# Kernel tuning notes

Measured on AMD Instinct MI355X. Metric: run time of the kernel, lower is better.

Reference implementation:

```python
import jax, jax.numpy as jnp
import numpy as np

B = 1048576          # batch size
ALPHA1, ALPHA2, ALPHA3 = 1.2566, 1.5, 0.9
S_STAR = 20.0
TAU = 4.0


def _f_matrix(a1, a2, a3):
    # fixed 6x6 dynamics matrix built by the i in {1,2} loop in CBF_Parameters
    f = jnp.zeros((6, 6), jnp.float32)
    f = f.at[2, 1].set(1.0).at[2, 3].set(-1.0)
    f = f.at[3, 1].set(a3).at[3, 2].set(a1).at[3, 3].set(-a2)
    f = f.at[4, 3].set(1.0).at[4, 5].set(-1.0)
    f = f.at[5, 3].set(a3).at[5, 4].set(a1).at[5, 5].set(-a2)
    return f


def setup_inputs() -> dict:
    key = jax.random.key(0)
    ks = jax.random.split(key, 7)
    z = jax.random.normal(ks[0], (B, 6), jnp.float32)
    tilde_vh = jnp.zeros((1,), jnp.float32)  # unused in forward (dead code in source)
    W1 = jax.random.normal(ks[1], (50, 6), jnp.float32) * 0.3
    b1 = jax.random.normal(ks[2], (50,), jnp.float32) * 0.1
    W2 = jax.random.normal(ks[3], (100, 50), jnp.float32) * 0.1
    b2 = jax.random.normal(ks[4], (100,), jnp.float32) * 0.1
    W3 = jax.random.normal(ks[5], (5, 100), jnp.float32) * 0.1
    b3 = jax.random.normal(ks[6], (5,), jnp.float32) * 0.1
    return dict(z=z, tilde_vh=tilde_vh, W1=W1, b1=b1, W2=W2, b2=b2, W3=W3, b3=b3)


def reference(z, tilde_vh, W1, b1, W2, b2, W3, b3):
    # tiny MLP, no activations (faithful to fc3(fc2(fc1(z))))
    u = ((z @ W1.T + b1) @ W2.T + b2) @ W3.T + b3        # (B, 5)
    p1, p2, p3 = u[:, 1], u[:, 2], u[:, 3]

    # faithful: torch reshape (row-major reinterpret), not transpose
    X = z.reshape(6, -1)                                  # (6, B)
    f = _f_matrix(ALPHA1, ALPHA2, ALPHA3)
    fX = f @ X                                            # (6, B)

    # index == 2 constraint (while loop body never runs: delta_b[1]=tau != 0)
    d2 = jnp.zeros(6, jnp.float32).at[1].set(TAU).at[2].set(1.0).at[3].set(-TAU)
    eta1 = X[2] + S_STAR - TAU * (X[3] - X[1])            # (B,)
    bb1 = d2 @ fX + p1 * eta1                             # (B,)

    # index == 3 constraint (while loop runs exactly once: d3[1]==0 -> d3u[1]=tau*alpha3)
    d3 = jnp.zeros(6, jnp.float32).at[3].set(TAU).at[4].set(1.0).at[5].set(-TAU)
    d3u = d3 @ f                                          # one f-multiplication
    eta2a = X[4] + S_STAR - TAU * (X[5] - X[3])           # (B,)
    eta2b = d3u @ X                                       # (B,)
    bb2 = d3u @ fX + p2 * eta2a + p3 * eta2b              # (B,)

    A = jnp.stack([-d2[1], -d3u[1]])                      # (2,) constraint normals
    h = jnp.stack([bb1, bb2], axis=1)                     # (B, 2)

    # per-sample 1-D QP: min 0.25*x^2 - u0*x  s.t. A_i * x <= h_i  (Q = 0.5)
    x_unc = 2.0 * u[:, 0]
    ratios = h / A                                        # (B, 2)
    neg_inf = jnp.float32(-1e30)
    pos_inf = jnp.float32(1e30)
    lb = jnp.max(jnp.where(A < 0, ratios, neg_inf), axis=1)
    ub = jnp.min(jnp.where(A > 0, ratios, pos_inf), axis=1)
    return jnp.clip(x_unc, lb, ub)[:, None]               # (B, 1)
```

## Files before the change

### kernel.cpp

```cpp
#include <hip/hip_runtime.h>

#define ALPHA1 1.2566f
#define ALPHA2 1.5f
#define ALPHA3 0.9f
#define S_STAR 20.0f
#define TAU    4.0f

constexpr int TPB = 256;

__global__ __launch_bounds__(TPB) void fused_kernel(
        const float* __restrict__ z,
        const float* __restrict__ W1, const float* __restrict__ b1,
        const float* __restrict__ W2, const float* __restrict__ b2,
        const float* __restrict__ W3, const float* __restrict__ b3,
        float* __restrict__ out, long long B) {
    __shared__ float Vs[4][52];
    __shared__ float Ms[4][6];
    __shared__ float cs[4];
    const int tid = threadIdx.x;

    if (tid < 200) {
        const int m = tid / 50, h = tid % 50;
        float s = 0.f;
        #pragma unroll 10
        for (int i = 0; i < 100; ++i)
            s = fmaf(W3[m * 100 + i], W2[i * 50 + h], s);
        Vs[m][h] = s;
    }
    __syncthreads();
    if (tid < 24) {
        const int m = tid / 6, k = tid % 6;
        float s = 0.f;
        #pragma unroll 10
        for (int h = 0; h < 50; ++h)
            s = fmaf(Vs[m][h], W1[h * 6 + k], s);
        Ms[m][k] = s;
    } else if (tid < 28) {
        const int m = tid - 24;
        float s = b3[m];
        #pragma unroll 10
        for (int i = 0; i < 100; ++i)
            s = fmaf(W3[m * 100 + i], b2[i], s);
        #pragma unroll 10
        for (int h = 0; h < 50; ++h)
            s = fmaf(Vs[m][h], b1[h], s);
        cs[m] = s;
    }
    __syncthreads();

    float M[4][6], c[4];
    #pragma unroll
    for (int m = 0; m < 4; ++m) {
        #pragma unroll
        for (int k = 0; k < 6; ++k) M[m][k] = Ms[m][k];
        c[m] = cs[m];
    }

    const float g1 = TAU * ALPHA3;
    const float g2 = TAU * ALPHA1;
    const float g3 = 1.f - TAU * ALPHA2 - TAU * ALPHA3;
    const float g4 = -TAU * ALPHA1;
    const float g5 = TAU * ALPHA2 - 1.f;

    #pragma unroll
    for (int s2 = 0; s2 < 2; ++s2) {
        const long long j0 =
            ((long long)blockIdx.x * (2 * TPB) + s2 * TPB + tid) * 4;

        float zz[24];
        const float4* zr = (const float4*)(z + j0 * 6);
        #pragma unroll
        for (int v = 0; v < 6; ++v) {
            const float4 q = zr[v];
            zz[4 * v + 0] = q.x; zz[4 * v + 1] = q.y;
            zz[4 * v + 2] = q.z; zz[4 * v + 3] = q.w;
        }

        float X[6][4];
        #pragma unroll
        for (int i = 0; i < 6; ++i) {
            const float4 q = *(const float4*)(z + (long long)i * B + j0);
            X[i][0] = q.x; X[i][1] = q.y; X[i][2] = q.z; X[i][3] = q.w;
        }

        float4 o;
        float* op = &o.x;
        #pragma unroll
        for (int r = 0; r < 4; ++r) {
            float u[4];
            #pragma unroll
            for (int m = 0; m < 4; ++m) {
                float s = c[m];
                #pragma unroll
                for (int k = 0; k < 6; ++k) s = fmaf(M[m][k], zz[r * 6 + k], s);
                u[m] = s;
            }
            const float x1 = X[1][r], x2 = X[2][r], x3 = X[3][r];
            const float x4 = X[4][r], x5 = X[5][r];

            const float fx2 = x1 - x3;
            const float fx3 = ALPHA3 * x1 + ALPHA1 * x2 - ALPHA2 * x3;
            const float fx4 = x3 - x5;
            const float fx5 = ALPHA3 * x3 + ALPHA1 * x4 - ALPHA2 * x5;

            const float eta1 = x2 + S_STAR - TAU * (x3 - x1);
            const float bb1  = (fx2 - TAU * fx3) + u[1] * eta1;

            const float eta2a = x4 + S_STAR - TAU * (x5 - x3);
            const float eta2b = g1 * x1 + g2 * x2 + g3 * x3 + g4 * x4 + g5 * x5;
            const float d3ufX = g2 * fx2 + g3 * fx3 + g4 * fx4 + g5 * fx5;
            const float bb2   = d3ufX + u[2] * eta2a + u[3] * eta2b;

            const float r1 = bb1 / (-TAU);
            const float r2 = bb2 / (-(TAU * ALPHA3));
            const float lb = fmaxf(r1, r2);
            const float xu = 2.f * u[0];
            op[r] = fminf(fmaxf(xu, lb), 1e30f);
        }
        *(float4*)(out + j0) = o;
    }
}

extern "C" void kernel_launch(void* const* d_in, const int* in_sizes, int n_in,
                              void* d_out, int out_size, void* d_ws, size_t ws_size,
                              hipStream_t stream) {
    const float* z  = (const float*)d_in[0];
    const float* W1 = (const float*)d_in[2];
    const float* b1 = (const float*)d_in[3];
    const float* W2 = (const float*)d_in[4];
    const float* b2 = (const float*)d_in[5];
    const float* W3 = (const float*)d_in[6];
    const float* b3 = (const float*)d_in[7];
    float* out = (float*)d_out;

    const long long B = (long long)in_sizes[0] / 6;

    const int blocks = (int)(B / (4LL * 2 * TPB));
    fused_kernel<<<blocks, TPB, 0, stream>>>(z, W1, b1, W2, b2, W3, b3, out, B);
}
```

Before: 93.05 us.

## Prefetch z before weight folding, stage rows via LDS, parallelize weight collapse

Each block now issues its global loads of z (both the row-major and the reshaped column views) before it computes the collapsed MLP weights, so memory latency overlaps the per-block weight folding. The row-major loads are made coalesced by staging them through a shared-memory slab. The weight collapse becomes a single parallel pass over all 256 threads with wave shuffle reductions, replacing the earlier serial two-stage chain. Block work is halved to one group of 4 rows per thread, and divisions become multiplies by reciprocals. The cost is extra shared memory (about 24KB per block), which may reduce occupancy, and twice as many blocks, each repeating the weight fold.

```diff
diff --git a/kernel.cpp b/kernel.cpp
--- a/kernel.cpp
+++ b/kernel.cpp
@@ -7,6 +7,8 @@
 #define TAU    4.0f
 
 constexpr int TPB = 256;
+constexpr int JPT = 4;
+constexpr int JPB = TPB * JPT;
 
 __global__ __launch_bounds__(TPB) void fused_kernel(
         const float* __restrict__ z,
@@ -14,38 +16,62 @@
         const float* __restrict__ W2, const float* __restrict__ b2,
         const float* __restrict__ W3, const float* __restrict__ b3,
         float* __restrict__ out, long long B) {
-    __shared__ float Vs[4][52];
+    __shared__ float w1s[300];
+    __shared__ float b1s[50];
+    __shared__ float b2s[100];
     __shared__ float Ms[4][6];
     __shared__ float cs[4];
+    __shared__ float slab[JPB * 6];
+
     const int tid = threadIdx.x;
+    const long long blockBase = (long long)blockIdx.x * JPB;
 
-    if (tid < 200) {
-        const int m = tid / 50, h = tid % 50;
-        float s = 0.f;
-        #pragma unroll 10
-        for (int i = 0; i < 100; ++i)
-            s = fmaf(W3[m * 100 + i], W2[i * 50 + h], s);
-        Vs[m][h] = s;
+    float4 s4[6];
+    const float4* zr4 = (const float4*)(z + blockBase * 6);
+    #pragma unroll
+    for (int it = 0; it < 6; ++it) s4[it] = zr4[it * TPB + tid];
+
+    const long long j0 = blockBase + (long long)tid * JPT;
+    float4 col[6];
+    #pragma unroll
+    for (int i = 0; i < 6; ++i)
+        col[i] = *(const float4*)(z + (long long)i * B + j0);
+
+    for (int idx = tid; idx < 300; idx += TPB) w1s[idx] = W1[idx];
+    if (tid < 50) b1s[tid] = b1[tid];
+    else if (tid >= 64 && tid < 164) b2s[tid - 64] = b2[tid - 64];
+    __syncthreads();
+
+    {
+        const int m    = tid >> 6;
+        const int lane = tid & 63;
+        float acc[8] = {0.f, 0.f, 0.f, 0.f, 0.f, 0.f, 0.f, 0.f};
+        for (int p = lane; p < 5000; p += 64) {
+            const int i = p / 50;
+            const int h = p - i * 50;
+            const float w3 = W3[m * 100 + i];
+            const float t  = w3 * W2[p];
+            acc[6] = fmaf(t, b1s[h], acc[6]);
+            #pragma unroll
+            for (int k = 0; k < 6; ++k)
+                acc[k] = fmaf(t, w1s[h * 6 + k], acc[k]);
+            if (h == 0) acc[7] = fmaf(w3, b2s[i], acc[7]);
+        }
+        #pragma unroll
+        for (int off = 32; off > 0; off >>= 1) {
+            #pragma unroll
+            for (int r = 0; r < 8; ++r) acc[r] += __shfl_xor(acc[r], off);
+        }
+        if (lane == 0) {
+            #pragma unroll
+            for (int k = 0; k < 6; ++k) Ms[m][k] = acc[k];
+            cs[m] = b3[m] + acc[6] + acc[7];
+        }
     }
-    __syncthreads();
-    if (tid < 24) {
-        const int m = tid / 6, k = tid % 6;
-        float s = 0.f;
-        #pragma unroll 10
-        for (int h = 0; h < 50; ++h)
-            s = fmaf(Vs[m][h], W1[h * 6 + k], s);
-        Ms[m][k] = s;
-    } else if (tid < 28) {
-        const int m = tid - 24;
-        float s = b3[m];
-        #pragma unroll 10
-        for (int i = 0; i < 100; ++i)
-            s = fmaf(W3[m * 100 + i], b2[i], s);
-        #pragma unroll 10
-        for (int h = 0; h < 50; ++h)
-            s = fmaf(Vs[m][h], b1[h], s);
-        cs[m] = s;
-    }
+
+    #pragma unroll
+    for (int it = 0; it < 6; ++it)
+        *(float4*)(&slab[(it * TPB + tid) * 4]) = s4[it];
     __syncthreads();
 
     float M[4][6], c[4];
@@ -61,64 +87,52 @@
     const float g3 = 1.f - TAU * ALPHA2 - TAU * ALPHA3;
     const float g4 = -TAU * ALPHA1;
     const float g5 = TAU * ALPHA2 - 1.f;
+    const float invA1 = -0.25f;
+    const float invA2 = -1.f / (TAU * ALPHA3);
 
+    float zz[24];
     #pragma unroll
-    for (int s2 = 0; s2 < 2; ++s2) {
-        const long long j0 =
-            ((long long)blockIdx.x * (2 * TPB) + s2 * TPB + tid) * 4;
+    for (int v = 0; v < 6; ++v) {
+        const float4 q = *(const float4*)(&slab[tid * 24 + v * 4]);
+        zz[4 * v + 0] = q.x; zz[4 * v + 1] = q.y;
+        zz[4 * v + 2] = q.z; zz[4 * v + 3] = q.w;
+    }
 
-        float zz[24];
-        const float4* zr = (const float4*)(z + j0 * 6);
+    float4 o;
+    float* op = &o.x;
+    const float* cp[6] = {&col[0].x, &col[1].x, &col[2].x,
+                          &col[3].x, &col[4].x, &col[5].x};
+    #pragma unroll
+    for (int r = 0; r < 4; ++r) {
+        float u[4];
         #pragma unroll
-        for (int v = 0; v < 6; ++v) {
-            const float4 q = zr[v];
-            zz[4 * v + 0] = q.x; zz[4 * v + 1] = q.y;
-            zz[4 * v + 2] = q.z; zz[4 * v + 3] = q.w;
+        for (int m = 0; m < 4; ++m) {
+            float s = c[m];
+            #pragma unroll
+            for (int k = 0; k < 6; ++k) s = fmaf(M[m][k], zz[r * 6 + k], s);
+            u[m] = s;
         }
+        const float x1 = cp[1][r], x2 = cp[2][r], x3 = cp[3][r];
+        const float x4 = cp[4][r], x5 = cp[5][r];
 
-        float X[6][4];
-        #pragma unroll
-        for (int i = 0; i < 6; ++i) {
-            const float4 q = *(const float4*)(z + (long long)i * B + j0);
-            X[i][0] = q.x; X[i][1] = q.y; X[i][2] = q.z; X[i][3] = q.w;
-        }
+        const float fx2 = x1 - x3;
+        const float fx3 = ALPHA3 * x1 + ALPHA1 * x2 - ALPHA2 * x3;
+        const float fx4 = x3 - x5;
+        const float fx5 = ALPHA3 * x3 + ALPHA1 * x4 - ALPHA2 * x5;
 
-        float4 o;
-        float* op = &o.x;
-        #pragma unroll
-        for (int r = 0; r < 4; ++r) {
-            float u[4];
-            #pragma unroll
-            for (int m = 0; m < 4; ++m) {
-                float s = c[m];
-                #pragma unroll
-                for (int k = 0; k < 6; ++k) s = fmaf(M[m][k], zz[r * 6 + k], s);
-                u[m] = s;
-            }
-            const float x1 = X[1][r], x2 = X[2][r], x3 = X[3][r];
-            const float x4 = X[4][r], x5 = X[5][r];
+        const float eta1 = x2 + S_STAR - TAU * (x3 - x1);
+        const float bb1  = (fx2 - TAU * fx3) + u[1] * eta1;
 
-            const float fx2 = x1 - x3;
-            const float fx3 = ALPHA3 * x1 + ALPHA1 * x2 - ALPHA2 * x3;
-            const float fx4 = x3 - x5;
-            const float fx5 = ALPHA3 * x3 + ALPHA1 * x4 - ALPHA2 * x5;
+        const float eta2a = x4 + S_STAR - TAU * (x5 - x3);
+        const float eta2b = g1 * x1 + g2 * x2 + g3 * x3 + g4 * x4 + g5 * x5;
+        const float d3ufX = g2 * fx2 + g3 * fx3 + g4 * fx4 + g5 * fx5;
+        const float bb2   = d3ufX + u[2] * eta2a + u[3] * eta2b;
 
-            const float eta1 = x2 + S_STAR - TAU * (x3 - x1);
-            const float bb1  = (fx2 - TAU * fx3) + u[1] * eta1;
-
-            const float eta2a = x4 + S_STAR - TAU * (x5 - x3);
-            const float eta2b = g1 * x1 + g2 * x2 + g3 * x3 + g4 * x4 + g5 * x5;
-            const float d3ufX = g2 * fx2 + g3 * fx3 + g4 * fx4 + g5 * fx5;
-            const float bb2   = d3ufX + u[2] * eta2a + u[3] * eta2b;
-
-            const float r1 = bb1 / (-TAU);
-            const float r2 = bb2 / (-(TAU * ALPHA3));
-            const float lb = fmaxf(r1, r2);
-            const float xu = 2.f * u[0];
-            op[r] = fminf(fmaxf(xu, lb), 1e30f);
-        }
-        *(float4*)(out + j0) = o;
+        const float lb = fmaxf(bb1 * invA1, bb2 * invA2);
+        const float xu = 2.f * u[0];
+        op[r] = fminf(fmaxf(xu, lb), 1e30f);
     }
+    *(float4*)(out + j0) = o;
 }
 
 extern "C" void kernel_launch(void* const* d_in, const int* in_sizes, int n_in,
@@ -134,7 +148,7 @@
     float* out = (float*)d_out;
 
     const long long B = (long long)in_sizes[0] / 6;
+    const int blocks = (int)(B / JPB);
 
-    const int blocks = (int)(B / (4LL * 2 * TPB));
     fused_kernel<<<blocks, TPB, 0, stream>>>(z, W1, b1, W2, b2, W3, b3, out, B);
 }
```

Result: slower. 120.8 us (+29.8%).

## Issue input loads before weight folding and shrink per-thread work

Applied to the files above, without the earlier changes.

Moves each thread's global loads of z ahead of the per-block MLP weight-folding prologue, so memory latency overlaps the prologue. The prologue is reordered to compute W2·[W1|b1] first with 100 threads, then W3 on top with 28 threads, instead of the earlier order that left most threads idle. Per-thread work drops from 8 samples to 2, which quadruples the block count and adds launch_bounds occupancy hints. Divisions are replaced by multiplication with precomputed reciprocals. The trade-off is that every block now repeats the weight-folding prologue, and there are four times as many blocks.

```diff
diff --git a/kernel.cpp b/kernel.cpp
--- a/kernel.cpp
+++ b/kernel.cpp
@@ -7,118 +7,118 @@
 #define TAU    4.0f
 
 constexpr int TPB = 256;
+constexpr int JPT = 2;
+constexpr int JPB = TPB * JPT;
 
-__global__ __launch_bounds__(TPB) void fused_kernel(
+__global__ __launch_bounds__(TPB, 8) void fused_kernel(
         const float* __restrict__ z,
         const float* __restrict__ W1, const float* __restrict__ b1,
         const float* __restrict__ W2, const float* __restrict__ b2,
         const float* __restrict__ W3, const float* __restrict__ b3,
         float* __restrict__ out, long long B) {
-    __shared__ float Vs[4][52];
-    __shared__ float Ms[4][6];
-    __shared__ float cs[4];
+    __shared__ float W1e[50][8];
+    __shared__ float T[100][8];
+    __shared__ float Mc[4][8];
+
     const int tid = threadIdx.x;
+    const long long j0 = ((long long)blockIdx.x * TPB + tid) * JPT;
 
-    if (tid < 200) {
-        const int m = tid / 50, h = tid % 50;
-        float s = 0.f;
-        #pragma unroll 10
-        for (int i = 0; i < 100; ++i)
-            s = fmaf(W3[m * 100 + i], W2[i * 50 + h], s);
-        Vs[m][h] = s;
-    }
-    __syncthreads();
-    if (tid < 24) {
-        const int m = tid / 6, k = tid % 6;
-        float s = 0.f;
-        #pragma unroll 10
-        for (int h = 0; h < 50; ++h)
-            s = fmaf(Vs[m][h], W1[h * 6 + k], s);
-        Ms[m][k] = s;
-    } else if (tid < 28) {
-        const int m = tid - 24;
-        float s = b3[m];
-        #pragma unroll 10
-        for (int i = 0; i < 100; ++i)
-            s = fmaf(W3[m * 100 + i], b2[i], s);
-        #pragma unroll 10
-        for (int h = 0; h < 50; ++h)
-            s = fmaf(Vs[m][h], b1[h], s);
-        cs[m] = s;
+    const float4 r0 = *(const float4*)(z + j0 * 6);
+    const float4 r1 = *(const float4*)(z + j0 * 6 + 4);
+    const float4 r2 = *(const float4*)(z + j0 * 6 + 8);
+    const float2 c1 = *(const float2*)(z + 1 * B + j0);
+    const float2 c2 = *(const float2*)(z + 2 * B + j0);
+    const float2 c3 = *(const float2*)(z + 3 * B + j0);
+    const float2 c4 = *(const float2*)(z + 4 * B + j0);
+    const float2 c5 = *(const float2*)(z + 5 * B + j0);
+
+    if (tid < 50) {
+        const float2 a = *(const float2*)(W1 + tid * 6);
+        const float2 b = *(const float2*)(W1 + tid * 6 + 2);
+        const float2 d = *(const float2*)(W1 + tid * 6 + 4);
+        W1e[tid][0] = a.x; W1e[tid][1] = a.y;
+        W1e[tid][2] = b.x; W1e[tid][3] = b.y;
+        W1e[tid][4] = d.x; W1e[tid][5] = d.y;
+        W1e[tid][6] = b1[tid];
     }
     __syncthreads();
 
-    float M[4][6], c[4];
-    #pragma unroll
-    for (int m = 0; m < 4; ++m) {
+    if (tid < 100) {
+        float acc[7] = {0.f, 0.f, 0.f, 0.f, 0.f, 0.f, 0.f};
+        acc[6] = b2[tid];
+        const float2* wrow = (const float2*)(W2 + tid * 50);
+        #pragma unroll 5
+        for (int hh = 0; hh < 25; ++hh) {
+            const float2 w = wrow[hh];
+            const int h = 2 * hh;
+            #pragma unroll
+            for (int k = 0; k < 7; ++k)
+                acc[k] = fmaf(w.y, W1e[h + 1][k], fmaf(w.x, W1e[h][k], acc[k]));
+        }
         #pragma unroll
-        for (int k = 0; k < 6; ++k) M[m][k] = Ms[m][k];
-        c[m] = cs[m];
+        for (int k = 0; k < 7; ++k) T[tid][k] = acc[k];
     }
+    __syncthreads();
+
+    if (tid < 28) {
+        const int m = tid / 7, k = tid % 7;
+        float s = (k == 6) ? b3[m] : 0.f;
+        #pragma unroll 10
+        for (int i = 0; i < 100; ++i)
+            s = fmaf(W3[m * 100 + i], T[i][k], s);
+        Mc[m][k] = s;
+    }
+    __syncthreads();
 
     const float g1 = TAU * ALPHA3;
     const float g2 = TAU * ALPHA1;
     const float g3 = 1.f - TAU * ALPHA2 - TAU * ALPHA3;
     const float g4 = -TAU * ALPHA1;
     const float g5 = TAU * ALPHA2 - 1.f;
+    const float invA1 = -0.25f;
+    const float invA2 = -1.f / (TAU * ALPHA3);
 
+    const float zz[12] = {r0.x, r0.y, r0.z, r0.w,
+                          r1.x, r1.y, r1.z, r1.w,
+                          r2.x, r2.y, r2.z, r2.w};
+
+    float2 o;
+    float* op = &o.x;
     #pragma unroll
-    for (int s2 = 0; s2 < 2; ++s2) {
-        const long long j0 =
-            ((long long)blockIdx.x * (2 * TPB) + s2 * TPB + tid) * 4;
+    for (int r = 0; r < 2; ++r) {
+        float u[4];
+        #pragma unroll
+        for (int m = 0; m < 4; ++m) {
+            float s = Mc[m][6];
+            #pragma unroll
+            for (int k = 0; k < 6; ++k)
+                s = fmaf(Mc[m][k], zz[r * 6 + k], s);
+            u[m] = s;
+        }
+        const float x1 = r ? c1.y : c1.x;
+        const float x2 = r ? c2.y : c2.x;
+        const float x3 = r ? c3.y : c3.x;
+        const float x4 = r ? c4.y : c4.x;
+        const float x5 = r ? c5.y : c5.x;
 
-        float zz[24];
-        const float4* zr = (const float4*)(z + j0 * 6);
-        #pragma unroll
-        for (int v = 0; v < 6; ++v) {
-            const float4 q = zr[v];
-            zz[4 * v + 0] = q.x; zz[4 * v + 1] = q.y;
-            zz[4 * v + 2] = q.z; zz[4 * v + 3] = q.w;
-        }
+        const float fx2 = x1 - x3;
+        const float fx3 = ALPHA3 * x1 + ALPHA1 * x2 - ALPHA2 * x3;
+        const float fx4 = x3 - x5;
+        const float fx5 = ALPHA3 * x3 + ALPHA1 * x4 - ALPHA2 * x5;
 
-        float X[6][4];
-        #pragma unroll
-        for (int i = 0; i < 6; ++i) {
-            const float4 q = *(const float4*)(z + (long long)i * B + j0);
-            X[i][0] = q.x; X[i][1] = q.y; X[i][2] = q.z; X[i][3] = q.w;
-        }
+        const float eta1 = x2 + S_STAR - TAU * (x3 - x1);
+        const float bb1  = (fx2 - TAU * fx3) + u[1] * eta1;
 
-        float4 o;
-        float* op = &o.x;
-        #pragma unroll
-        for (int r = 0; r < 4; ++r) {
-            float u[4];
-            #pragma unroll
-            for (int m = 0; m < 4; ++m) {
-                float s = c[m];
-                #pragma unroll
-                for (int k = 0; k < 6; ++k) s = fmaf(M[m][k], zz[r * 6 + k], s);
-                u[m] = s;
-            }
-            const float x1 = X[1][r], x2 = X[2][r], x3 = X[3][r];
-            const float x4 = X[4][r], x5 = X[5][r];
+        const float eta2a = x4 + S_STAR - TAU * (x5 - x3);
+        const float eta2b = g1 * x1 + g2 * x2 + g3 * x3 + g4 * x4 + g5 * x5;
+        const float d3ufX = g2 * fx2 + g3 * fx3 + g4 * fx4 + g5 * fx5;
+        const float bb2   = d3ufX + u[2] * eta2a + u[3] * eta2b;
 
-            const float fx2 = x1 - x3;
-            const float fx3 = ALPHA3 * x1 + ALPHA1 * x2 - ALPHA2 * x3;
-            const float fx4 = x3 - x5;
-            const float fx5 = ALPHA3 * x3 + ALPHA1 * x4 - ALPHA2 * x5;
-
-            const float eta1 = x2 + S_STAR - TAU * (x3 - x1);
-            const float bb1  = (fx2 - TAU * fx3) + u[1] * eta1;
-
-            const float eta2a = x4 + S_STAR - TAU * (x5 - x3);
-            const float eta2b = g1 * x1 + g2 * x2 + g3 * x3 + g4 * x4 + g5 * x5;
-            const float d3ufX = g2 * fx2 + g3 * fx3 + g4 * fx4 + g5 * fx5;
-            const float bb2   = d3ufX + u[2] * eta2a + u[3] * eta2b;
-
-            const float r1 = bb1 / (-TAU);
-            const float r2 = bb2 / (-(TAU * ALPHA3));
-            const float lb = fmaxf(r1, r2);
-            const float xu = 2.f * u[0];
-            op[r] = fminf(fmaxf(xu, lb), 1e30f);
-        }
-        *(float4*)(out + j0) = o;
+        const float lb = fmaxf(bb1 * invA1, bb2 * invA2);
+        const float xu = 2.f * u[0];
+        op[r] = fminf(fmaxf(xu, lb), 1e30f);
     }
+    *(float2*)(out + j0) = o;
 }
 
 extern "C" void kernel_launch(void* const* d_in, const int* in_sizes, int n_in,
@@ -134,7 +134,7 @@
     float* out = (float*)d_out;
 
     const long long B = (long long)in_sizes[0] / 6;
+    const int blocks = (int)(B / JPB);
 
-    const int blocks = (int)(B / (4LL * 2 * TPB));
     fused_kernel<<<blocks, TPB, 0, stream>>>(z, W1, b1, W2, b2, W3, b3, out, B);
 }
```

Result: no change. 92.45 us (-0.6%).
